# Kernel optimization log

Measured on AMD Instinct MI355X. Metric: run time of the kernel, lower is better.

The kernel has to match this reference:

```python
import jax, jax.numpy as jnp
import numpy as np

NEG_SLOPE = 0.2


def _add_self_loops(edge_index, n_nodes):
    loop = jnp.arange(n_nodes, dtype=edge_index.dtype)
    src = jnp.concatenate([edge_index[0], loop])
    dst = jnp.concatenate([edge_index[1], loop])
    return src, dst


def _gat_layer(x, src, dst, W, a_src, a_dst, b):
    # PyG GATConv, heads=1: h = x @ W; e_ij = LeakyReLU(a_src.h_j + a_dst.h_i)
    # softmax over incoming edges of each dst node, then weighted aggregate.
    n = x.shape[0]
    h = x @ W                      # [N, d]
    s = h @ a_src                  # [N] per-source score
    t = h @ a_dst                  # [N] per-dest score
    e = jax.nn.leaky_relu(s[src] + t[dst], NEG_SLOPE)          # [E]
    m = jax.ops.segment_max(e, dst, num_segments=n)            # stable softmax
    ex = jnp.exp(e - m[dst])
    denom = jax.ops.segment_sum(ex, dst, num_segments=n)
    alpha = ex / denom[dst]                                     # [E]
    out = jax.ops.segment_sum(h[src] * alpha[:, None], dst, num_segments=n)
    return out + b


def setup_inputs() -> dict:
    key = jax.random.key(0)
    ks = jax.random.split(key, 16)
    N, E, d = 50000, 800000, 64
    sc = 1.0 / np.sqrt(d)
    inp = {
        "x": jax.random.normal(ks[0], (N, d), dtype=jnp.float32),
        "edge_index": jax.random.randint(ks[1], (2, E), 0, N, dtype=jnp.int64),
    }
    for i, layer in enumerate((1, 2, 3)):
        inp[f"W{layer}"] = jax.random.normal(ks[2 + 4 * i], (d, d), dtype=jnp.float32) * sc
        inp[f"a_src{layer}"] = jax.random.normal(ks[3 + 4 * i], (d,), dtype=jnp.float32) * sc
        inp[f"a_dst{layer}"] = jax.random.normal(ks[4 + 4 * i], (d,), dtype=jnp.float32) * sc
        inp[f"b{layer}"] = jnp.zeros((d,), dtype=jnp.float32)
    return inp


def reference(x, edge_index, W1, a_src1, a_dst1, b1, W2, a_src2, a_dst2, b2,
              W3, a_src3, a_dst3, b3):
    n = x.shape[0]
    src, dst = _add_self_loops(edge_index, n)
    x = jax.nn.relu(_gat_layer(x, src, dst, W1, a_src1, a_dst1, b1))
    x = jax.nn.relu(_gat_layer(x, src, dst, W2, a_src2, a_dst2, b2))
    x = jax.nn.relu(_gat_layer(x, src, dst, W3, a_src3, a_dst3, b3))
    return x
```

## Files before the change

kernel.cpp:

```cpp
#include <hip/hip_runtime.h>
#include <hip/hip_fp16.h>

#define NEG_SLOPE 0.2f
#define MAXDEG 64

__device__ __forceinline__ float readlane_f(float v, int l) {
    return __uint_as_float(__builtin_amdgcn_readlane(__float_as_uint(v), l));
}
__device__ __forceinline__ int readlane_i(int v, int l) {
    return __builtin_amdgcn_readlane(v, l);
}


__device__ __forceinline__ void bucket_body(const int* __restrict__ ei, int E,
                                            int* __restrict__ cnt, int* __restrict__ slots,
                                            int bid) {
    int t = bid * 256 + threadIdx.x;
    int base = t * 8;
    if (base >= E) return;
    int s[8], d[8];
    if (base + 7 < E) {
        int4 sa = *(const int4*)(ei + base);
        int4 sb = *(const int4*)(ei + base + 4);
        int4 da = *(const int4*)(ei + E + base);
        int4 db = *(const int4*)(ei + E + base + 4);
        s[0]=sa.x; s[1]=sa.y; s[2]=sa.z; s[3]=sa.w; s[4]=sb.x; s[5]=sb.y; s[6]=sb.z; s[7]=sb.w;
        d[0]=da.x; d[1]=da.y; d[2]=da.z; d[3]=da.w; d[4]=db.x; d[5]=db.y; d[6]=db.z; d[7]=db.w;
    } else {
        #pragma unroll
        for (int j = 0; j < 8; j++) {
            int e = base + j;
            if (e < E) { s[j] = ei[e]; d[j] = ei[E + e]; }
            else       { s[j] = -1;    d[j] = -1; }
        }
    }
    int pos[8];
    #pragma unroll
    for (int j = 0; j < 8; j++)
        pos[j] = (d[j] >= 0) ? atomicAdd(&cnt[d[j]], 1) : MAXDEG;
    #pragma unroll
    for (int j = 0; j < 8; j++)
        if (pos[j] < MAXDEG)
            __builtin_nontemporal_store(s[j], &slots[(size_t)d[j] * MAXDEG + pos[j]]);
}


__device__ __forceinline__ void gemm_body(const float* __restrict__ x, const float* __restrict__ W,
                                          const float* __restrict__ a_src, const float* __restrict__ a_dst,
                                          __half* __restrict__ h16, float* __restrict__ sv,
                                          float* __restrict__ tv, int n, int bid) {
    __shared__ float Wl[64 * 64];
    __shared__ float Xl[64 * 68];
    int tid = threadIdx.x;
    int n0 = bid * 64;

    #pragma unroll
    for (int r = 0; r < 4; r++) {
        int f = tid + r * 256;
        int k = f >> 4, c = (f & 15) * 4;
        *(float4*)(&Wl[k * 64 + c]) = *(const float4*)(W + (size_t)f * 4);
    }
    #pragma unroll
    for (int r = 0; r < 4; r++) {
        int f = tid + r * 256;
        int node = f >> 4, k = (f & 15) * 4;
        float4 xv = make_float4(0.f, 0.f, 0.f, 0.f);
        if (n0 + node < n) xv = *(const float4*)(x + (size_t)(n0 + node) * 64 + k);
        Xl[(k + 0) * 68 + node] = xv.x;
        Xl[(k + 1) * 68 + node] = xv.y;
        Xl[(k + 2) * 68 + node] = xv.z;
        Xl[(k + 3) * 68 + node] = xv.w;
    }
    __syncthreads();

    int tx = tid & 15, ty = tid >> 4;
    float acc[4][4] = {{0.f}};
    #pragma unroll 16
    for (int k = 0; k < 64; k++) {
        float4 xv = *(const float4*)(&Xl[k * 68 + ty * 4]);
        float4 wv = *(const float4*)(&Wl[k * 64 + tx * 4]);
        acc[0][0] += xv.x * wv.x; acc[0][1] += xv.x * wv.y; acc[0][2] += xv.x * wv.z; acc[0][3] += xv.x * wv.w;
        acc[1][0] += xv.y * wv.x; acc[1][1] += xv.y * wv.y; acc[1][2] += xv.y * wv.z; acc[1][3] += xv.y * wv.w;
        acc[2][0] += xv.z * wv.x; acc[2][1] += xv.z * wv.y; acc[2][2] += xv.z * wv.z; acc[2][3] += xv.z * wv.w;
        acc[3][0] += xv.w * wv.x; acc[3][1] += xv.w * wv.y; acc[3][2] += xv.w * wv.z; acc[3][3] += xv.w * wv.w;
    }

    float4 as4 = *(const float4*)(a_src + tx * 4);
    float4 ad4 = *(const float4*)(a_dst + tx * 4);
    #pragma unroll
    for (int j = 0; j < 4; j++) {
        int node = n0 + ty * 4 + j;
        float sp = acc[j][0] * as4.x + acc[j][1] * as4.y + acc[j][2] * as4.z + acc[j][3] * as4.w;
        float tp = acc[j][0] * ad4.x + acc[j][1] * ad4.y + acc[j][2] * ad4.z + acc[j][3] * ad4.w;
        #pragma unroll
        for (int o = 1; o < 16; o <<= 1) {
            sp += __shfl_xor(sp, o);
            tp += __shfl_xor(tp, o);
        }
        if (node < n) {
            union { __half2 h2[2]; uint2 u; } pk;
            pk.h2[0] = __floats2half2_rn(acc[j][0], acc[j][1]);
            pk.h2[1] = __floats2half2_rn(acc[j][2], acc[j][3]);
            *(uint2*)(h16 + (size_t)node * 64 + tx * 4) = pk.u;
            if (tx == 0) { sv[node] = sp; tv[node] = tp; }
        }
    }
}

__global__ __launch_bounds__(256) void k_fused1(const int* __restrict__ ei, int E,
                                                int* __restrict__ cnt, int* __restrict__ slots,
                                                const float* __restrict__ x, const float* __restrict__ W,
                                                const float* __restrict__ a_src, const float* __restrict__ a_dst,
                                                __half* __restrict__ h16, float* __restrict__ sv,
                                                float* __restrict__ tv, int n, int gB) {
    int bid = blockIdx.x;
    if (bid < gB) bucket_body(ei, E, cnt, slots, bid);
    else          gemm_body(x, W, a_src, a_dst, h16, sv, tv, n, bid - gB);
}

__global__ __launch_bounds__(256) void k_gemm(const float* __restrict__ x, const float* __restrict__ W,
                                              const float* __restrict__ a_src, const float* __restrict__ a_dst,
                                              __half* __restrict__ h16, float* __restrict__ sv,
                                              float* __restrict__ tv, int n) {
    gemm_body(x, W, a_src, a_dst, h16, sv, tv, n, blockIdx.x);
}


#define GATHER8(K)                                                            \
    {                                                                         \
        float e0 = readlane_f(ex, (K) + 0), e1 = readlane_f(ex, (K) + 1);     \
        float e2 = readlane_f(ex, (K) + 2), e3 = readlane_f(ex, (K) + 3);     \
        float e4 = readlane_f(ex, (K) + 4), e5 = readlane_f(ex, (K) + 5);     \
        float e6 = readlane_f(ex, (K) + 6), e7 = readlane_f(ex, (K) + 7);     \
        int s0 = readlane_i(sid, (K) + 0), s1 = readlane_i(sid, (K) + 1);     \
        int s2 = readlane_i(sid, (K) + 2), s3 = readlane_i(sid, (K) + 3);     \
        int s4 = readlane_i(sid, (K) + 4), s5 = readlane_i(sid, (K) + 5);     \
        int s6 = readlane_i(sid, (K) + 6), s7 = readlane_i(sid, (K) + 7);     \
        float v0 = __half2float(h16[(size_t)s0 * 64 + lane]);                 \
        float v1 = __half2float(h16[(size_t)s1 * 64 + lane]);                 \
        float v2 = __half2float(h16[(size_t)s2 * 64 + lane]);                 \
        float v3 = __half2float(h16[(size_t)s3 * 64 + lane]);                 \
        float v4 = __half2float(h16[(size_t)s4 * 64 + lane]);                 \
        float v5 = __half2float(h16[(size_t)s5 * 64 + lane]);                 \
        float v6 = __half2float(h16[(size_t)s6 * 64 + lane]);                 \
        float v7 = __half2float(h16[(size_t)s7 * 64 + lane]);                 \
        acc0 += e0 * v0; acc1 += e1 * v1; acc2 += e2 * v2; acc3 += e3 * v3;   \
        acc0 += e4 * v4; acc1 += e5 * v5; acc2 += e6 * v6; acc3 += e7 * v7;   \
    }

__global__ __launch_bounds__(1024) void k_agg(const __half* __restrict__ h16, const float* __restrict__ sv,
                                              const float* __restrict__ tv, const int* __restrict__ cnt,
                                              const int* __restrict__ slots, const float* __restrict__ bias,
                                              float* __restrict__ xout, int n) {
    int wid = (blockIdx.x * 1024 + threadIdx.x) >> 6;
    int lane = threadIdx.x & 63;
    if (wid >= n) return;
    int deg = cnt[wid];
    if (deg > 63) deg = 63;
    int ecount = deg + 1;
    float tn = tv[wid];

    int sid = 0;
    bool valid = lane < ecount;
    if (valid) sid = (lane == deg) ? wid : slots[(size_t)wid * MAXDEG + lane];
    float ss = valid ? sv[sid] : 0.f;
    float ev = ss + tn;
    ev = (ev > 0.f) ? ev : NEG_SLOPE * ev;
    float ex = valid ? __expf(ev) : 0.f;

    float denom = ex;
    #pragma unroll
    for (int o = 1; o < 64; o <<= 1) denom += __shfl_xor(denom, o);

    float acc0 = 0.f, acc1 = 0.f, acc2 = 0.f, acc3 = 0.f;
    if (ecount <= 24) {
        GATHER8(0) GATHER8(8) GATHER8(16)
    } else {
        int cnt8 = (ecount + 7) & ~7;
        for (int k = 0; k < cnt8; k += 8) GATHER8(k)
    }

    float o = (acc0 + acc1) + (acc2 + acc3);
    o = o / denom + bias[lane];
    xout[(size_t)wid * 64 + lane] = fmaxf(o, 0.f);
}


extern "C" void kernel_launch(void* const* d_in, const int* in_sizes, int n_in,
                              void* d_out, int out_size, void* d_ws, size_t ws_size,
                              hipStream_t stream) {
    const float* x0 = (const float*)d_in[0];
    const int* ei = (const int*)d_in[1];
    const float* Wp[3]    = {(const float*)d_in[2],  (const float*)d_in[6],  (const float*)d_in[10]};
    const float* asp[3]   = {(const float*)d_in[3],  (const float*)d_in[7],  (const float*)d_in[11]};
    const float* adp[3]   = {(const float*)d_in[4],  (const float*)d_in[8],  (const float*)d_in[12]};
    const float* bp[3]    = {(const float*)d_in[5],  (const float*)d_in[9],  (const float*)d_in[13]};

    int N = in_sizes[0] / 64;
    int E = in_sizes[1] / 2;

    char* wp = (char*)d_ws;
    auto alloc = [&wp](size_t bytes) {
        char* p = wp;
        wp += (bytes + 255) & ~(size_t)255;
        return p;
    };
    float*  bufA   = (float*)alloc((size_t)N * 64 * sizeof(float));
    __half* h16    = (__half*)alloc((size_t)N * 64 * sizeof(__half));
    int*    slots  = (int*)alloc((size_t)N * MAXDEG * sizeof(int));
    float*  sArr   = (float*)alloc((size_t)N * sizeof(float));
    float*  tArr   = (float*)alloc((size_t)N * sizeof(float));
    int*    cntArr = (int*)alloc((size_t)N * sizeof(int));

    hipMemsetAsync(cntArr, 0, (size_t)N * sizeof(int), stream);

    int gB = ((E + 7) / 8 + 255) / 256;
    int gG = (N + 63) / 64;
    int gAgg = (N + 15) / 16;

    k_fused1<<<gB + gG, 256, 0, stream>>>(ei, E, cntArr, slots,
                                          x0, Wp[0], asp[0], adp[0], h16, sArr, tArr, N, gB);
    k_agg<<<gAgg, 1024, 0, stream>>>(h16, sArr, tArr, cntArr, slots, bp[0], bufA, N);
    k_gemm<<<gG, 256, 0, stream>>>(bufA, Wp[1], asp[1], adp[1], h16, sArr, tArr, N);
    k_agg<<<gAgg, 1024, 0, stream>>>(h16, sArr, tArr, cntArr, slots, bp[1], bufA, N);
    k_gemm<<<gG, 256, 0, stream>>>(bufA, Wp[2], asp[2], adp[2], h16, sArr, tArr, N);
    k_agg<<<gAgg, 1024, 0, stream>>>(h16, sArr, tArr, cntArr, slots, bp[2], (float*)d_out, N);
}
```

Baseline: 175.8 us.

## Partition edge bucketing by destination range across 8 block replicas

Each edge window is now processed by 8 blocks, and each block handles only the edges whose destination falls in its eighth of the node range. The apparent intent is to confine each block's atomics and slot writes to a narrower address region, presumably matching blocks to XCD partitions for locality. The cost is that every block re-reads its whole edge window, so edge-index traffic is read eight times, and eight times as many bucketing blocks are launched.

```diff
diff --git a/kernel.cpp b/kernel.cpp
--- a/kernel.cpp
+++ b/kernel.cpp
@@ -12,11 +12,13 @@
 }
 
 
-__device__ __forceinline__ void bucket_body(const int* __restrict__ ei, int E,
+__device__ __forceinline__ void bucket_body(const int* __restrict__ ei, int E, int ps,
                                             int* __restrict__ cnt, int* __restrict__ slots,
                                             int bid) {
-    int t = bid * 256 + threadIdx.x;
-    int base = t * 8;
+    int w = bid >> 3;
+    int p = bid & 7;
+    int lo = p * ps, hi = lo + ps;
+    int base = (w * 256 + (int)threadIdx.x) * 8;
     if (base >= E) return;
     int s[8], d[8];
     if (base + 7 < E) {
@@ -31,17 +33,18 @@
         for (int j = 0; j < 8; j++) {
             int e = base + j;
             if (e < E) { s[j] = ei[e]; d[j] = ei[E + e]; }
-            else       { s[j] = -1;    d[j] = -1; }
-        }
-    }
-    int pos[8];
-    #pragma unroll
-    for (int j = 0; j < 8; j++)
-        pos[j] = (d[j] >= 0) ? atomicAdd(&cnt[d[j]], 1) : MAXDEG;
-    #pragma unroll
-    for (int j = 0; j < 8; j++)
-        if (pos[j] < MAXDEG)
-            __builtin_nontemporal_store(s[j], &slots[(size_t)d[j] * MAXDEG + pos[j]]);
+            else       { s[j] = 0;     d[j] = -1; }
+        }
+    }
+    #pragma unroll
+    for (int j = 0; j < 8; j++) {
+        bool mine = (d[j] >= lo) && (d[j] < hi);
+        if (mine) {
+            int pos = atomicAdd(&cnt[d[j]], 1);
+            if (pos < MAXDEG)
+                __builtin_nontemporal_store(s[j], &slots[(size_t)d[j] * MAXDEG + pos]);
+        }
+    }
 }
 
 
@@ -107,14 +110,14 @@
     }
 }
 
-__global__ __launch_bounds__(256) void k_fused1(const int* __restrict__ ei, int E,
+__global__ __launch_bounds__(256) void k_fused1(const int* __restrict__ ei, int E, int ps,
                                                 int* __restrict__ cnt, int* __restrict__ slots,
                                                 const float* __restrict__ x, const float* __restrict__ W,
                                                 const float* __restrict__ a_src, const float* __restrict__ a_dst,
                                                 __half* __restrict__ h16, float* __restrict__ sv,
                                                 float* __restrict__ tv, int n, int gB) {
     int bid = blockIdx.x;
-    if (bid < gB) bucket_body(ei, E, cnt, slots, bid);
+    if (bid < gB) bucket_body(ei, E, ps, cnt, slots, bid);
     else          gemm_body(x, W, a_src, a_dst, h16, sv, tv, n, bid - gB);
 }
 
@@ -214,11 +217,13 @@
 
     hipMemsetAsync(cntArr, 0, (size_t)N * sizeof(int), stream);
 
-    int gB = ((E + 7) / 8 + 255) / 256;
+    int ps = (N + 7) / 8;
+    int nWin = (E + 2047) / 2048;
+    int gB = nWin * 8;
     int gG = (N + 63) / 64;
     int gAgg = (N + 15) / 16;
 
-    k_fused1<<<gB + gG, 256, 0, stream>>>(ei, E, cntArr, slots,
+    k_fused1<<<gB + gG, 256, 0, stream>>>(ei, E, ps, cntArr, slots,
                                           x0, Wp[0], asp[0], adp[0], h16, sArr, tArr, N, gB);
     k_agg<<<gAgg, 1024, 0, stream>>>(h16, sArr, tArr, cntArr, slots, bp[0], bufA, N);
     k_gemm<<<gG, 256, 0, stream>>>(bufA, Wp[1], asp[1], adp[1], h16, sArr, tArr, N);
```

Measured after the change: 172.3 us. 2.0% less time.
